# Performance work log

Measured on AMD Instinct MI355X. Metric: run time of the kernel, lower is better.

## Reference

```python
import math
import jax, jax.numpy as jnp
import numpy as np

N, C, T, V = 32, 256, 128, 25
DK, DV, NH = 64, 256, 8
DKH, DVH = DK // NH, DV // NH
EPS = 1e-5


def _spatial_pe(channels, joints):
    # spatial positional encoding: position = joint index, same for all frames
    pos = jnp.arange(joints, dtype=jnp.float32)  # (V,)
    div = jnp.exp(jnp.arange(0, channels, 2, dtype=jnp.float32) * (-math.log(10000.0) / channels))
    ang = pos[:, None] * div[None, :]  # (V, C/2)
    pe = jnp.stack([jnp.sin(ang), jnp.cos(ang)], axis=-1).reshape(joints, channels)  # interleave sin/cos
    return pe.T  # (C, V)


def _qkv_heads(inp, qkv_w, qkv_b):
    # inp: (N, T, C, V); 1x1 conv == channel GEMM
    qkv = jnp.einsum('oc,ntcv->ntov', qkv_w, inp) + qkv_b[None, None, :, None]
    q = qkv[:, :, :DK].reshape(N, T, NH, DKH, V) * (DKH ** -0.5)
    k = qkv[:, :, DK:2 * DK].reshape(N, T, NH, DKH, V)
    g = qkv[:, :, 2 * DK:3 * DK].reshape(N, T, NH, DKH, V)
    v = qkv[:, :, 3 * DK:].reshape(N, T, NH, DVH, V)
    return q, k, g, v


def setup_inputs() -> dict:
    key = jax.random.key(0)
    ks = jax.random.split(key, 3)
    return {
        'x': jax.random.normal(ks[0], (N, C, T, V), dtype=jnp.float32),
        'qkv_w': jax.random.normal(ks[1], (3 * DK + DV, C), dtype=jnp.float32) * 0.02,
        'qkv_b': jnp.zeros((3 * DK + DV,), dtype=jnp.float32),
        'attn_w': jax.random.normal(ks[2], (DV, DV), dtype=jnp.float32) * 0.02,
        'attn_b': jnp.zeros((DV,), dtype=jnp.float32),
        'dbn_gamma': jnp.ones((C * V,), dtype=jnp.float32),
        'dbn_beta': jnp.zeros((C * V,), dtype=jnp.float32),
        'bn_gamma': jnp.ones((DV,), dtype=jnp.float32),
        'bn_beta': jnp.zeros((DV,), dtype=jnp.float32),
    }


def reference(x, qkv_w, qkv_b, attn_w, attn_b, dbn_gamma, dbn_beta, bn_gamma, bn_beta):
    x_sum = x
    pe = _spatial_pe(C, V)  # (C, V)
    pos = x + pe[None, :, None, :]  # broadcast over N, T

    # data_bn: BatchNorm1d over C*V features (training mode, batch stats over N and T)
    xr = x.transpose(0, 1, 3, 2).reshape(N, C * V, T)
    mu = xr.mean(axis=(0, 2))
    var = xr.var(axis=(0, 2))
    xr = (xr - mu[None, :, None]) * jax.lax.rsqrt(var + EPS)[None, :, None]
    xr = xr * dbn_gamma[None, :, None] + dbn_beta[None, :, None]
    xn = xr.reshape(N, C, V, T).transpose(0, 1, 3, 2)  # (N, C, T, V)

    xa = xn.transpose(0, 2, 1, 3)   # (N, T, C, V)
    pa = pos.transpose(0, 2, 1, 3)  # (N, T, C, V)

    q, k, g, v = _qkv_heads(xa, qkv_w, qkv_b)
    pq, pk, _, _ = _qkv_heads(pa, qkv_w, qkv_b)

    mu_q = q.mean(-1, keepdims=True)          # (N,T,Nh,dkh,1)
    qc = q - mu_q
    pairwise = jnp.einsum('nthdv,nthdw->nthvw', qc, k)    # (N,T,Nh,V,V)
    unary = jnp.einsum('nthdv,nthdw->nthvw', mu_q, g)     # (N,T,Nh,1,V)
    lp = jnp.einsum('nthdv,nthdw->nthvw', pq, pk)         # (N,T,Nh,V,V)

    weights = jnp.tanh(pairwise + lp) + jnp.tanh(unary + lp)
    attn = jnp.einsum('nthvw,nthew->nthev', weights, v)   # (N,T,Nh,dvh,V)
    attn = attn.reshape(N, T, DV, V)
    attn = jnp.einsum('oe,ntev->ntov', attn_w, attn) + attn_b[None, None, :, None]
    y = attn.transpose(0, 2, 1, 3) + x_sum  # skip (in_c == out_c)

    # bn: BatchNorm2d over out_c (training mode)
    mu2 = y.mean(axis=(0, 2, 3))
    var2 = y.var(axis=(0, 2, 3))
    y = (y - mu2[None, :, None, None]) * jax.lax.rsqrt(var2 + EPS)[None, :, None, None]
    y = y * bn_gamma[None, :, None, None] + bn_beta[None, :, None, None]
    return jax.nn.relu(y)
```

## Files before the change

### kernel.cpp

```cpp
#include <hip/hip_runtime.h>
#include <hip/hip_bf16.h>
#include <math.h>

#define N_   32
#define C_   256
#define T_   128
#define V_   25
#define CTV  (C_ * T_ * V_)
#define TV   (T_ * V_)
#define EPS_ 1e-5f
#define S_Q  0.35355339059327373f
#define NCOPY 64

typedef __attribute__((ext_vector_type(8))) short bf16x8;
typedef __attribute__((ext_vector_type(4))) float f32x4;
typedef __attribute__((ext_vector_type(4))) unsigned short u16x4;

__device__ inline ushort f2b(float f) {
    __hip_bfloat16 h = __float2bfloat16(f);
    return *reinterpret_cast<ushort*>(&h);
}
__device__ inline float b2f(ushort u) {
    __hip_bfloat16 h;
    *reinterpret_cast<ushort*>(&h) = u;
    return __bfloat162float(h);
}
__device__ inline float tanh_fast(float x) {
    float xc = fminf(fmaxf(x, -12.f), 12.f);
    float e = __expf(xc + xc);
    return (e - 1.f) * __builtin_amdgcn_rcpf(e + 1.f);
}
#define LD8(p) (*(const bf16x8*)(p))
#define MFMA16(a, b, c) __builtin_amdgcn_mfma_f32_16x16x32_bf16(a, b, c, 0, 0, 0)

__device__ inline int qtswz(int v, int col) {
    return v * 320 + ((((col >> 3)) ^ (v & 7)) << 3) + (col & 7);
}
__device__ inline int qvswz(int e, int w) {
    return e * 32 + (((w >> 3) ^ (e & 3)) << 3) + (w & 7);
}
__device__ inline int bswz(int v, int c) {
    return v * 256 + ((((c >> 3) ^ (v & 7)) << 3) | (c & 7));
}

__global__ void prep_kernel(const float* __restrict__ qkv_w,
                            const float* __restrict__ attn_w,
                            ushort* __restrict__ Wq, ushort* __restrict__ Wa,
                            float* __restrict__ pe, float* __restrict__ bins) {
    int idx = blockIdx.x * blockDim.x + threadIdx.x;
    int stride = gridDim.x * blockDim.x;
    for (int i = idx; i < 448 * 256; i += stride) {
        float w = qkv_w[i];
        if (i < 64 * 256) w *= S_Q;
        Wq[i] = f2b(w);
    }
    for (int i = idx; i < 256 * 256; i += stride) Wa[i] = f2b(attn_w[i]);
    for (int i = idx; i < C_ * V_; i += stride) {
        int c = i / V_, v = i - c * V_;
        int j2 = c & ~1;
        float ang = (float)v * expf(-logf(10000.0f) * (float)j2 / (float)C_);
        pe[i] = (c & 1) ? cosf(ang) : sinf(ang);
    }
    for (int i = idx; i < NCOPY * 512; i += stride) bins[i] = 0.f;
}

__global__ __launch_bounds__(1024) void dbn_kernel(const float* __restrict__ x,
                                                   const float* __restrict__ gamma,
                                                   const float* __restrict__ beta,
                                                   float* __restrict__ a_scale,
                                                   float* __restrict__ a_shift) {
    __shared__ float pgS[32][25], pgQ[32][25];
    int c = blockIdx.x;
    int tid = threadIdx.x, g = tid >> 5, l = tid & 31;
    float s = 0.f, s2 = 0.f;
    if (l < 25) {
        const float* base = x + (size_t)g * CTV + c * TV + l;
        #pragma unroll 8
        for (int t = 0; t < 128; ++t) {
            float v = base[t * 25];
            s += v; s2 += v * v;
        }
        pgS[g][l] = s; pgQ[g][l] = s2;
    }
    __syncthreads();
    if (tid < 25) {
        float S = 0.f, Q = 0.f;
        #pragma unroll
        for (int g2 = 0; g2 < 32; ++g2) { S += pgS[g2][tid]; Q += pgQ[g2][tid]; }
        float inv = 1.0f / 4096.0f;
        float mean = S * inv, var = Q * inv - mean * mean;
        int f = c * 25 + tid;
        float sc = rsqrtf(var + EPS_) * gamma[f];
        a_scale[f] = sc;
        a_shift[f] = beta[f] - mean * sc;
    }
}

__global__ void mkbias_kernel(const ushort* __restrict__ Wq,
                              const float* __restrict__ qkv_b,
                              const float* __restrict__ a_shift,
                              const float* __restrict__ pe,
                              float* __restrict__ bias2, float* __restrict__ peproj) {
    int id = blockIdx.x * 256 + threadIdx.x;
    if (id < 11200) {
        int o = id / 25, v = id - o * 25;
        float acc = qkv_b[o] * (o < 64 ? S_Q : 1.f);
        for (int c = 0; c < 256; ++c)
            acc = fmaf(b2f(Wq[o * 256 + c]), a_shift[c * 25 + v], acc);
        bias2[id] = acc;
    } else if (id < 14400) {
        int id2 = id - 11200;
        int r = id2 / 25, v = id2 - r * 25;
        float acc = qkv_b[r] * (r < 64 ? S_Q : 1.f);
        for (int c = 0; c < 256; ++c)
            acc = fmaf(b2f(Wq[r * 256 + c]), pe[c * 25 + v], acc);
        peproj[id2] = acc;
    }
}

__global__ void b2sum_kernel(const float* __restrict__ bias2,
                             float* __restrict__ bias2sum) {
    int o = threadIdx.x;
    float s = 0.f;
    #pragma unroll
    for (int v = 0; v < 25; ++v) s += bias2[o * 25 + v];
    bias2sum[o] = s;
}

__global__ __launch_bounds__(512, 4) void fused_kernel(
        const float* __restrict__ x,
        const ushort* __restrict__ Wq,
        const float* __restrict__ bias2, const float* __restrict__ peproj,
        const float* __restrict__ a_scale, const float* __restrict__ bias2sum,
        const ushort* __restrict__ Wa, const float* __restrict__ attn_b,
        float* __restrict__ out, float* __restrict__ bins) {
    __shared__ __align__(16) char smem[53376];
    ushort* Braw = (ushort*)smem;
    ushort* Bxn  = (ushort*)(smem + 16384);
    ushort* qkvT = (ushort*)(smem + 32768);
    ushort* qkvV = (ushort*)smem;
    ushort* aT   = (ushort*)(smem + 16384);
    ushort* pbuf = (ushort*)(smem + 32768);
    ushort* qmub = (ushort*)(smem + 53248);

    int n = blockIdx.x >> 7, t = blockIdx.x & 127;
    int tid = threadIdx.x, wave = tid >> 6, lane = tid & 63;
    int lr = lane & 15, lg = lane >> 4;
    const float* xp = x + (size_t)n * CTV + t * V_;
    float* outp = out + (size_t)n * CTV + t * V_;
    float* mybins = bins + (blockIdx.x & (NCOPY - 1)) * 512;
    const f32x4 zacc = {0.f, 0.f, 0.f, 0.f};
    const bf16x8 zero8 = {0, 0, 0, 0, 0, 0, 0, 0};

    float b2s[4] = {0.f, 0.f, 0.f, 0.f};
    if (wave < 4) {
        #pragma unroll
        for (int i2 = 0; i2 < 4; ++i2)
            b2s[i2] = bias2sum[wave * 16 + lg * 4 + i2];
    }

    {
        float xv[13], sc[13];
        #pragma unroll
        for (int j = 0; j < 13; ++j) {
            int i = tid + j * 512;
            if (i < 6400) {
                int c = i / 25, v = i - c * 25;
                xv[j] = xp[c * TV + v];
                sc[j] = a_scale[i];
            }
        }
        #pragma unroll
        for (int j = 0; j < 13; ++j) {
            int i = tid + j * 512;
            if (i < 6400) {
                int c = i / 25, v = i - c * 25;
                int off = bswz(v, c);
                Braw[off] = f2b(xv[j]);
                Bxn[off]  = f2b(xv[j] * sc[j]);
            }
        }
        for (int i = tid; i < 448; i += 512) {
            int v = 25 + (i >> 6), c = (i & 63) * 4;
            u16x4 z4 = {0, 0, 0, 0};
            *(u16x4*)(Braw + v * 256 + c) = z4;
            *(u16x4*)(Bxn + v * 256 + c) = z4;
        }
    }
    __syncthreads();

    {
        const ushort* Arow = Wq + (wave * 16 + lr) * 256;
        f32x4 a0 = zacc, a1 = zacc;
        #pragma unroll
        for (int kk = 0; kk < 8; ++kk) {
            int k0 = kk * 32 + lg * 8;
            int oct = (((k0 >> 3) ^ (lr & 7)) << 3);
            bf16x8 a  = LD8(Arow + k0);
            bf16x8 b0 = LD8(Braw + lr * 256 + oct);
            bf16x8 b1 = LD8(Braw + (16 + lr) * 256 + oct);
            a0 = MFMA16(a, b0, a0);
            a1 = MFMA16(a, b1, a1);
        }
        int rb = wave * 16 + lg * 4;
        u16x4 r0, r1;
        #pragma unroll
        for (int i2 = 0; i2 < 4; ++i2) {
            int r = rb + i2;
            r0[i2] = f2b(a0[i2] + peproj[r * 25 + lr]);
            r1[i2] = (lr < 9) ? f2b(a1[i2] + peproj[r * 25 + 16 + lr]) : (ushort)0;
        }
        *(u16x4*)(qkvT + qtswz(lr, 192 + rb)) = r0;
        *(u16x4*)(qkvT + qtswz(16 + lr, 192 + rb)) = r1;
    }
    __syncthreads();

    {
        int myTiles = (wave < 4) ? 4 : 3;
        f32x4 acc[4][2];
        #pragma unroll
        for (int i = 0; i < 4; ++i) { acc[i][0] = zacc; acc[i][1] = zacc; }
        #pragma unroll
        for (int kk = 0; kk < 8; ++kk) {
            int k0 = kk * 32 + lg * 8;
            int oct = (((k0 >> 3) ^ (lr & 7)) << 3);
            bf16x8 b0 = LD8(Bxn + lr * 256 + oct);
            bf16x8 b1 = LD8(Bxn + (16 + lr) * 256 + oct);
            #pragma unroll
            for (int tt = 0; tt < 4; ++tt) {
                if (tt < myTiles) {
                    int mt = wave + tt * 8;
                    bf16x8 a = LD8(Wq + (mt * 16 + lr) * 256 + k0);
                    acc[tt][0] = MFMA16(a, b0, acc[tt][0]);
                    acc[tt][1] = MFMA16(a, b1, acc[tt][1]);
                }
            }
        }
        #pragma unroll
        for (int tt = 0; tt < 4; ++tt) {
            if (tt < myTiles) {
                int mt = wave + tt * 8;
                int ob = mt * 16 + lg * 4;
                if (mt < 4) {
                    u16x4 r0, r1;
                    #pragma unroll
                    for (int i2 = 0; i2 < 4; ++i2) {
                        int o = ob + i2;
                        float cs = acc[tt][0][i2] + ((lr < 9) ? acc[tt][1][i2] : 0.f);
                        #pragma unroll
                        for (int mm = 1; mm < 16; mm <<= 1)
                            cs += __shfl_xor(cs, mm, 64);
                        float mu = (cs + b2s[i2]) * 0.04f;
                        ushort mur = f2b(mu);
                        float muf = b2f(mur);
                        r0[i2] = f2b(acc[tt][0][i2] + bias2[o * 25 + lr] - muf);
                        r1[i2] = (lr < 9)
                            ? f2b(acc[tt][1][i2] + bias2[o * 25 + 16 + lr] - muf)
                            : (ushort)0;
                        if (lr == 0) qmub[o] = mur;
                    }
                    *(u16x4*)(qkvT + qtswz(lr, ob)) = r0;
                    *(u16x4*)(qkvT + qtswz(16 + lr, ob)) = r1;
                } else if (mt < 12) {
                    u16x4 r0, r1;
                    #pragma unroll
                    for (int i2 = 0; i2 < 4; ++i2) {
                        int o = ob + i2;
                        r0[i2] = f2b(acc[tt][0][i2] + bias2[o * 25 + lr]);
                        r1[i2] = (lr < 9)
                            ? f2b(acc[tt][1][i2] + bias2[o * 25 + 16 + lr])
                            : (ushort)0;
                    }
                    *(u16x4*)(qkvT + qtswz(lr, ob)) = r0;
                    *(u16x4*)(qkvT + qtswz(16 + lr, ob)) = r1;
                } else {
                    #pragma unroll
                    for (int i2 = 0; i2 < 4; ++i2) {
                        int o = ob + i2;
                        int e = o - 192;
                        qkvV[qvswz(e, lr)] = f2b(acc[tt][0][i2] + bias2[o * 25 + lr]);
                        qkvV[qvswz(e, 16 + lr)] = (lr < 9)
                            ? f2b(acc[tt][1][i2] + bias2[o * 25 + 16 + lr])
                            : (ushort)0;
                    }
                }
            }
        }
    }
    __syncthreads();

    int h = wave;
    bf16x8 mu8 = LD8(qmub + h * 8);
    bf16x8 aP1[2], aP2[2], bP1[2], bP2[2];
    #pragma unroll
    for (int mi = 0; mi < 2; ++mi) {
        int row = mi * 16 + lr, sx = row & 7;
        const ushort* rp = qkvT + row * 320;
        aP1[mi] = (lg == 0) ? LD8(rp + ((h ^ sx) << 3))
                : (lg == 1) ? LD8(rp + (((24 + h) ^ sx) << 3)) : zero8;
        aP2[mi] = (lg == 0) ? LD8(rp + (((24 + h) ^ sx) << 3))
                : (lg == 1) ? mu8 : zero8;
        bP1[mi] = (lg == 0) ? LD8(rp + (((8 + h) ^ sx) << 3))
                : (lg == 1) ? LD8(rp + (((32 + h) ^ sx) << 3)) : zero8;
        bP2[mi] = (lg == 0) ? LD8(rp + (((32 + h) ^ sx) << 3))
                : (lg == 1) ? LD8(rp + (((16 + h) ^ sx) << 3)) : zero8;
    }
    f32x4 p1[2][2], p2[2][2];
    #pragma unroll
    for (int mi = 0; mi < 2; ++mi)
        #pragma unroll
        for (int ni = 0; ni < 2; ++ni) {
            p1[mi][ni] = MFMA16(aP1[mi], bP1[ni], zacc);
            p2[mi][ni] = MFMA16(aP2[mi], bP2[ni], zacc);
        }
    __syncthreads();

    #pragma unroll
    for (int mi = 0; mi < 2; ++mi)
        #pragma unroll
        for (int ni = 0; ni < 2; ++ni) {
            int w = ni * 16 + lr;
            #pragma unroll
            for (int i2 = 0; i2 < 4; ++i2) {
                int v = mi * 16 + lg * 4 + i2;
                float tw = tanh_fast(p1[mi][ni][i2]) + tanh_fast(p2[mi][ni][i2]);
                pbuf[(h * 32 + v) * 40 + w] = (w < 25) ? f2b(tw) : (ushort)0;
            }
        }

    {
        bf16x8 aw[2], bv[2];
        #pragma unroll
        for (int mi = 0; mi < 2; ++mi)
            aw[mi] = LD8(pbuf + (h * 32 + mi * 16 + lr) * 40 + lg * 8);
        #pragma unroll
        for (int ni = 0; ni < 2; ++ni) {
            int e = h * 32 + ni * 16 + lr;
            bv[ni] = LD8(qkvV + e * 32 + ((lg ^ (e & 3)) << 3));
        }
        f32x4 at_[2][2];
        #pragma unroll
        for (int mi = 0; mi < 2; ++mi)
            #pragma unroll
            for (int ni = 0; ni < 2; ++ni)
                at_[mi][ni] = MFMA16(aw[mi], bv[ni], zacc);
        #pragma unroll
        for (int mi = 0; mi < 2; ++mi)
            #pragma unroll
            for (int ni = 0; ni < 2; ++ni)
                #pragma unroll
                for (int i2 = 0; i2 < 4; ++i2) {
                    int v = mi * 16 + lg * 4 + i2;
                    int e = h * 32 + ni * 16 + lr;
                    if (v < 25) aT[bswz(v, e)] = f2b(at_[mi][ni][i2]);
                }
    }
    __syncthreads();

    float sk0[2][4], sk1[2][4];
    #pragma unroll
    for (int tt = 0; tt < 2; ++tt)
        #pragma unroll
        for (int i2 = 0; i2 < 4; ++i2) {
            int o = (wave + tt * 8) * 16 + lg * 4 + i2;
            sk0[tt][i2] = xp[o * TV + lr];
            sk1[tt][i2] = (lr < 9) ? xp[o * TV + 16 + lr] : 0.f;
        }
    #pragma unroll
    for (int tt = 0; tt < 2; ++tt) {
        int o0 = (wave + tt * 8) * 16;
        const ushort* Arow = Wa + (o0 + lr) * 256;
        f32x4 a0 = zacc, a1 = zacc;
        #pragma unroll
        for (int kk = 0; kk < 8; ++kk) {
            int k0 = kk * 32 + lg * 8;
            int oct = (((k0 >> 3) ^ (lr & 7)) << 3);
            bf16x8 a  = LD8(Arow + k0);
            bf16x8 b0 = LD8(aT + lr * 256 + oct);
            bf16x8 b1 = LD8(aT + (16 + lr) * 256 + oct);
            a0 = MFMA16(a, b0, a0);
            a1 = MFMA16(a, b1, a1);
        }
        #pragma unroll
        for (int i2 = 0; i2 < 4; ++i2) {
            int o = o0 + lg * 4 + i2;
            float bias = attn_b[o];
            float v0 = a0[i2] + bias + sk0[tt][i2];
            outp[o * TV + lr] = v0;
            float v1 = 0.f;
            if (lr < 9) {
                v1 = a1[i2] + bias + sk1[tt][i2];
                outp[o * TV + 16 + lr] = v1;
            }
            float cs = v0 + v1, cq = v0 * v0 + v1 * v1;
            #pragma unroll
            for (int mm = 1; mm < 16; mm <<= 1) {
                cs += __shfl_xor(cs, mm, 64);
                cq += __shfl_xor(cq, mm, 64);
            }
            if (lr == 0) {
                atomicAdd(&mybins[o], cs);
                atomicAdd(&mybins[256 + o], cq);
            }
        }
    }
}

__global__ void bn2_final_kernel(const float* __restrict__ bins,
                                 const float* __restrict__ gamma,
                                 const float* __restrict__ beta,
                                 float* __restrict__ scale,
                                 float* __restrict__ shift) {
    int c = threadIdx.x;
    float s = 0.f, q = 0.f;
    for (int cp = 0; cp < NCOPY; ++cp) {
        s += bins[cp * 512 + c];
        q += bins[cp * 512 + 256 + c];
    }
    float inv = 1.0f / (float)(N_ * TV);
    float mean = s * inv;
    float var = q * inv - mean * mean;
    float sc = rsqrtf(var + EPS_) * gamma[c];
    scale[c] = sc;
    shift[c] = beta[c] - mean * sc;
}

__global__ void bn2_apply_kernel(float4* __restrict__ y,
                                 const float* __restrict__ scale,
                                 const float* __restrict__ shift) {
    const int total4 = N_ * CTV / 4;
    for (int i = blockIdx.x * blockDim.x + threadIdx.x; i < total4;
         i += gridDim.x * blockDim.x) {
        int c = (i / (TV / 4)) & 255;
        float4 v = y[i];
        float sc = scale[c], sh = shift[c];
        v.x = fmaxf(fmaf(v.x, sc, sh), 0.f);
        v.y = fmaxf(fmaf(v.y, sc, sh), 0.f);
        v.z = fmaxf(fmaf(v.z, sc, sh), 0.f);
        v.w = fmaxf(fmaf(v.w, sc, sh), 0.f);
        y[i] = v;
    }
}

extern "C" void kernel_launch(void* const* d_in, const int* in_sizes, int n_in,
                              void* d_out, int out_size, void* d_ws, size_t ws_size,
                              hipStream_t stream) {
    const float* x      = (const float*)d_in[0];
    const float* qkv_w  = (const float*)d_in[1];
    const float* qkv_b  = (const float*)d_in[2];
    const float* attn_w = (const float*)d_in[3];
    const float* attn_b = (const float*)d_in[4];
    const float* dbn_g  = (const float*)d_in[5];
    const float* dbn_b  = (const float*)d_in[6];
    const float* bn_g   = (const float*)d_in[7];
    const float* bn_b   = (const float*)d_in[8];
    float* out = (float*)d_out;

    char* ws = (char*)d_ws;
    ushort* Wq       = (ushort*)ws;
    ushort* Wa       = (ushort*)(ws + 229376);
    float*  pe       = (float*)(ws + 360448);
    float*  a_scale  = (float*)(ws + 386048);
    float*  a_shift  = (float*)(ws + 411648);
    float*  bias2    = (float*)(ws + 437248);
    float*  peproj   = (float*)(ws + 482048);
    float*  bias2sum = (float*)(ws + 494848);
    float*  bins     = (float*)(ws + 495104);
    float*  bn2_sc   = (float*)(ws + 626176);
    float*  bn2_sh   = (float*)(ws + 627200);

    prep_kernel<<<256, 256, 0, stream>>>(qkv_w, attn_w, Wq, Wa, pe, bins);
    dbn_kernel<<<C_, 1024, 0, stream>>>(x, dbn_g, dbn_b, a_scale, a_shift);
    mkbias_kernel<<<57, 256, 0, stream>>>(Wq, qkv_b, a_shift, pe, bias2, peproj);
    b2sum_kernel<<<1, 64, 0, stream>>>(bias2, bias2sum);
    fused_kernel<<<N_ * T_, 512, 0, stream>>>(x, Wq, bias2, peproj, a_scale,
                                              bias2sum, Wa, attn_b, out, bins);
    bn2_final_kernel<<<1, 256, 0, stream>>>(bins, bn_g, bn_b, bn2_sc, bn2_sh);
    bn2_apply_kernel<<<4096, 256, 0, stream>>>((float4*)out, bn2_sc, bn2_sh);
}
```

Measured before the change: 352.8 us.

## Prefetch GEMM weight fragments into registers and drop an intermediate barrier

Weight fragments for the PE projection GEMM are loaded into registers before the input staging phase. The QKV and output-projection GEMMs double-buffer their weight loads one k-step ahead, so global load latency overlaps with MFMA work. The barrier between the PE GEMM and the QKV GEMM is moved to after the QKV accumulation and before the epilogue writes into aliased shared memory. The input staging is also reorganised so each thread reads about 13 contiguous floats of one channel. The trade-off is a large rise in vector register use, which may lower occupancy, and the new per-thread access pattern for the input may coalesce less well.

```diff
diff --git a/kernel.cpp b/kernel.cpp
--- a/kernel.cpp
+++ b/kernel.cpp
@@ -151,7 +151,17 @@
     float* mybins = bins + (blockIdx.x & (NCOPY - 1)) * 512;
     const f32x4 zacc = {0.f, 0.f, 0.f, 0.f};
     const bf16x8 zero8 = {0, 0, 0, 0, 0, 0, 0, 0};
-
+    int myTiles = (wave < 4) ? 4 : 3;
+
+    bf16x8 apk[8];
+    const ushort* Arow0 = Wq + (wave * 16 + lr) * 256;
+    #pragma unroll
+    for (int kk = 0; kk < 8; ++kk) apk[kk] = LD8(Arow0 + kk * 32 + lg * 8);
+    bf16x8 acur[4];
+    #pragma unroll
+    for (int tt = 0; tt < 4; ++tt)
+        if (tt < myTiles)
+            acur[tt] = LD8(Wq + ((wave + tt * 8) * 16 + lr) * 256 + lg * 8);
     float b2s[4] = {0.f, 0.f, 0.f, 0.f};
     if (wave < 4) {
         #pragma unroll
@@ -160,47 +170,40 @@
     }
 
     {
+        int c = tid >> 1, half = tid & 1;
+        int v0 = half * 13, nv = 13 - half;
+        const float* xc = xp + c * TV + v0;
+        const float* scp = a_scale + c * 25 + v0;
         float xv[13], sc[13];
         #pragma unroll
-        for (int j = 0; j < 13; ++j) {
-            int i = tid + j * 512;
-            if (i < 6400) {
-                int c = i / 25, v = i - c * 25;
-                xv[j] = xp[c * TV + v];
-                sc[j] = a_scale[i];
-            }
-        }
-        #pragma unroll
-        for (int j = 0; j < 13; ++j) {
-            int i = tid + j * 512;
-            if (i < 6400) {
-                int c = i / 25, v = i - c * 25;
-                int off = bswz(v, c);
+        for (int j = 0; j < 13; ++j)
+            if (j < nv) { xv[j] = xc[j]; sc[j] = scp[j]; }
+        #pragma unroll
+        for (int j = 0; j < 13; ++j)
+            if (j < nv) {
+                int off = bswz(v0 + j, c);
                 Braw[off] = f2b(xv[j]);
                 Bxn[off]  = f2b(xv[j] * sc[j]);
             }
-        }
         for (int i = tid; i < 448; i += 512) {
-            int v = 25 + (i >> 6), c = (i & 63) * 4;
+            int v = 25 + (i >> 6), cz = (i & 63) * 4;
             u16x4 z4 = {0, 0, 0, 0};
-            *(u16x4*)(Braw + v * 256 + c) = z4;
-            *(u16x4*)(Bxn + v * 256 + c) = z4;
+            *(u16x4*)(Braw + v * 256 + cz) = z4;
+            *(u16x4*)(Bxn + v * 256 + cz) = z4;
         }
     }
     __syncthreads();
 
     {
-        const ushort* Arow = Wq + (wave * 16 + lr) * 256;
         f32x4 a0 = zacc, a1 = zacc;
         #pragma unroll
         for (int kk = 0; kk < 8; ++kk) {
             int k0 = kk * 32 + lg * 8;
             int oct = (((k0 >> 3) ^ (lr & 7)) << 3);
-            bf16x8 a  = LD8(Arow + k0);
             bf16x8 b0 = LD8(Braw + lr * 256 + oct);
             bf16x8 b1 = LD8(Braw + (16 + lr) * 256 + oct);
-            a0 = MFMA16(a, b0, a0);
-            a1 = MFMA16(a, b1, a1);
+            a0 = MFMA16(apk[kk], b0, a0);
+            a1 = MFMA16(apk[kk], b1, a1);
         }
         int rb = wave * 16 + lg * 4;
         u16x4 r0, r1;
@@ -213,15 +216,21 @@
         *(u16x4*)(qkvT + qtswz(lr, 192 + rb)) = r0;
         *(u16x4*)(qkvT + qtswz(16 + lr, 192 + rb)) = r1;
     }
-    __syncthreads();
-
+
+    f32x4 acc[4][2];
+    #pragma unroll
+    for (int i = 0; i < 4; ++i) { acc[i][0] = zacc; acc[i][1] = zacc; }
     {
-        int myTiles = (wave < 4) ? 4 : 3;
-        f32x4 acc[4][2];
-        #pragma unroll
-        for (int i = 0; i < 4; ++i) { acc[i][0] = zacc; acc[i][1] = zacc; }
+        bf16x8 anxt[4];
         #pragma unroll
         for (int kk = 0; kk < 8; ++kk) {
+            if (kk < 7) {
+                #pragma unroll
+                for (int tt = 0; tt < 4; ++tt)
+                    if (tt < myTiles)
+                        anxt[tt] = LD8(Wq + ((wave + tt * 8) * 16 + lr) * 256
+                                       + (kk + 1) * 32 + lg * 8);
+            }
             int k0 = kk * 32 + lg * 8;
             int oct = (((k0 >> 3) ^ (lr & 7)) << 3);
             bf16x8 b0 = LD8(Bxn + lr * 256 + oct);
@@ -229,60 +238,63 @@
             #pragma unroll
             for (int tt = 0; tt < 4; ++tt) {
                 if (tt < myTiles) {
-                    int mt = wave + tt * 8;
-                    bf16x8 a = LD8(Wq + (mt * 16 + lr) * 256 + k0);
-                    acc[tt][0] = MFMA16(a, b0, acc[tt][0]);
-                    acc[tt][1] = MFMA16(a, b1, acc[tt][1]);
+                    acc[tt][0] = MFMA16(acur[tt], b0, acc[tt][0]);
+                    acc[tt][1] = MFMA16(acur[tt], b1, acc[tt][1]);
                 }
             }
-        }
-        #pragma unroll
-        for (int tt = 0; tt < 4; ++tt) {
-            if (tt < myTiles) {
-                int mt = wave + tt * 8;
-                int ob = mt * 16 + lg * 4;
-                if (mt < 4) {
-                    u16x4 r0, r1;
+            #pragma unroll
+            for (int tt = 0; tt < 4; ++tt)
+                if (tt < myTiles) acur[tt] = anxt[tt];
+        }
+    }
+    __syncthreads();
+
+    #pragma unroll
+    for (int tt = 0; tt < 4; ++tt) {
+        if (tt < myTiles) {
+            int mt = wave + tt * 8;
+            int ob = mt * 16 + lg * 4;
+            if (mt < 4) {
+                u16x4 r0, r1;
+                #pragma unroll
+                for (int i2 = 0; i2 < 4; ++i2) {
+                    int o = ob + i2;
+                    float cs = acc[tt][0][i2] + ((lr < 9) ? acc[tt][1][i2] : 0.f);
                     #pragma unroll
-                    for (int i2 = 0; i2 < 4; ++i2) {
-                        int o = ob + i2;
-                        float cs = acc[tt][0][i2] + ((lr < 9) ? acc[tt][1][i2] : 0.f);
-                        #pragma unroll
-                        for (int mm = 1; mm < 16; mm <<= 1)
-                            cs += __shfl_xor(cs, mm, 64);
-                        float mu = (cs + b2s[i2]) * 0.04f;
-                        ushort mur = f2b(mu);
-                        float muf = b2f(mur);
-                        r0[i2] = f2b(acc[tt][0][i2] + bias2[o * 25 + lr] - muf);
-                        r1[i2] = (lr < 9)
-                            ? f2b(acc[tt][1][i2] + bias2[o * 25 + 16 + lr] - muf)
-                            : (ushort)0;
-                        if (lr == 0) qmub[o] = mur;
-                    }
-                    *(u16x4*)(qkvT + qtswz(lr, ob)) = r0;
-                    *(u16x4*)(qkvT + qtswz(16 + lr, ob)) = r1;
-                } else if (mt < 12) {
-                    u16x4 r0, r1;
-                    #pragma unroll
-                    for (int i2 = 0; i2 < 4; ++i2) {
-                        int o = ob + i2;
-                        r0[i2] = f2b(acc[tt][0][i2] + bias2[o * 25 + lr]);
-                        r1[i2] = (lr < 9)
-                            ? f2b(acc[tt][1][i2] + bias2[o * 25 + 16 + lr])
-                            : (ushort)0;
-                    }
-                    *(u16x4*)(qkvT + qtswz(lr, ob)) = r0;
-                    *(u16x4*)(qkvT + qtswz(16 + lr, ob)) = r1;
-                } else {
-                    #pragma unroll
-                    for (int i2 = 0; i2 < 4; ++i2) {
-                        int o = ob + i2;
-                        int e = o - 192;
-                        qkvV[qvswz(e, lr)] = f2b(acc[tt][0][i2] + bias2[o * 25 + lr]);
-                        qkvV[qvswz(e, 16 + lr)] = (lr < 9)
-                            ? f2b(acc[tt][1][i2] + bias2[o * 25 + 16 + lr])
-                            : (ushort)0;
-                    }
+                    for (int mm = 1; mm < 16; mm <<= 1)
+                        cs += __shfl_xor(cs, mm, 64);
+                    float mu = (cs + b2s[i2]) * 0.04f;
+                    ushort mur = f2b(mu);
+                    float muf = b2f(mur);
+                    r0[i2] = f2b(acc[tt][0][i2] + bias2[o * 25 + lr] - muf);
+                    r1[i2] = (lr < 9)
+                        ? f2b(acc[tt][1][i2] + bias2[o * 25 + 16 + lr] - muf)
+                        : (ushort)0;
+                    if (lr == 0) qmub[o] = mur;
+                }
+                *(u16x4*)(qkvT + qtswz(lr, ob)) = r0;
+                *(u16x4*)(qkvT + qtswz(16 + lr, ob)) = r1;
+            } else if (mt < 12) {
+                u16x4 r0, r1;
+                #pragma unroll
+                for (int i2 = 0; i2 < 4; ++i2) {
+                    int o = ob + i2;
+                    r0[i2] = f2b(acc[tt][0][i2] + bias2[o * 25 + lr]);
+                    r1[i2] = (lr < 9)
+                        ? f2b(acc[tt][1][i2] + bias2[o * 25 + 16 + lr])
+                        : (ushort)0;
+                }
+                *(u16x4*)(qkvT + qtswz(lr, ob)) = r0;
+                *(u16x4*)(qkvT + qtswz(16 + lr, ob)) = r1;
+            } else {
+                #pragma unroll
+                for (int i2 = 0; i2 < 4; ++i2) {
+                    int o = ob + i2;
+                    int e = o - 192;
+                    qkvV[qvswz(e, lr)] = f2b(acc[tt][0][i2] + bias2[o * 25 + lr]);
+                    qkvV[qvswz(e, 16 + lr)] = (lr < 9)
+                        ? f2b(acc[tt][1][i2] + bias2[o * 25 + 16 + lr])
+                        : (ushort)0;
                 }
             }
         }
@@ -371,15 +383,17 @@
         int o0 = (wave + tt * 8) * 16;
         const ushort* Arow = Wa + (o0 + lr) * 256;
         f32x4 a0 = zacc, a1 = zacc;
+        bf16x8 wac = LD8(Arow + lg * 8), wan;
         #pragma unroll
         for (int kk = 0; kk < 8; ++kk) {
+            if (kk < 7) wan = LD8(Arow + (kk + 1) * 32 + lg * 8);
             int k0 = kk * 32 + lg * 8;
             int oct = (((k0 >> 3) ^ (lr & 7)) << 3);
-            bf16x8 a  = LD8(Arow + k0);
             bf16x8 b0 = LD8(aT + lr * 256 + oct);
             bf16x8 b1 = LD8(aT + (16 + lr) * 256 + oct);
-            a0 = MFMA16(a, b0, a0);
-            a1 = MFMA16(a, b1, a1);
+            a0 = MFMA16(wac, b0, a0);
+            a1 = MFMA16(wac, b1, a1);
+            wac = wan;
         }
         #pragma unroll
         for (int i2 = 0; i2 < 4; ++i2) {
```

After: 374.4 us. 1.06x slower.

## Shrink LDS footprint by aliasing input buffers to raise block occupancy

Applied to the files above, without the earlier changes.

Cuts shared memory per block from about 53KB to 37KB. Instead of separate raw-x and normalized-x staging buffers, one buffer is reused: raw values are written first, then overwritten with scaled values after the first GEMM. V-projection results are kept in registers until the buffer is free, and extra barriers are added to order the aliased writes. This should let more 512-thread blocks fit per CU, at the cost of extra __syncthreads and more live registers (xv/sc arrays, accV), which could hit the launch-bounds register cap.

```diff
diff --git a/kernel.cpp b/kernel.cpp
--- a/kernel.cpp
+++ b/kernel.cpp
@@ -134,14 +134,13 @@
         const float* __restrict__ a_scale, const float* __restrict__ bias2sum,
         const ushort* __restrict__ Wa, const float* __restrict__ attn_b,
         float* __restrict__ out, float* __restrict__ bins) {
-    __shared__ __align__(16) char smem[53376];
-    ushort* Braw = (ushort*)smem;
-    ushort* Bxn  = (ushort*)(smem + 16384);
-    ushort* qkvT = (ushort*)(smem + 32768);
-    ushort* qkvV = (ushort*)smem;
-    ushort* aT   = (ushort*)(smem + 16384);
-    ushort* pbuf = (ushort*)(smem + 32768);
-    ushort* qmub = (ushort*)(smem + 53248);
+    __shared__ __align__(16) char smem[36992];
+    ushort* qkvT = (ushort*)smem;
+    ushort* pbuf = (ushort*)smem;
+    ushort* Bbuf = (ushort*)(smem + 20480);
+    ushort* qkvV = (ushort*)(smem + 20480);
+    ushort* aT   = (ushort*)(smem + 20480);
+    ushort* qmub = (ushort*)(smem + 36864);
 
     int n = blockIdx.x >> 7, t = blockIdx.x & 127;
     int tid = threadIdx.x, wave = tid >> 6, lane = tid & 63;
@@ -151,6 +150,7 @@
     float* mybins = bins + (blockIdx.x & (NCOPY - 1)) * 512;
     const f32x4 zacc = {0.f, 0.f, 0.f, 0.f};
     const bf16x8 zero8 = {0, 0, 0, 0, 0, 0, 0, 0};
+    int myTiles = (wave < 4) ? 4 : 3;
 
     float b2s[4] = {0.f, 0.f, 0.f, 0.f};
     if (wave < 4) {
@@ -159,8 +159,8 @@
             b2s[i2] = bias2sum[wave * 16 + lg * 4 + i2];
     }
 
+    float xv[13], sc[13];
     {
-        float xv[13], sc[13];
         #pragma unroll
         for (int j = 0; j < 13; ++j) {
             int i = tid + j * 512;
@@ -175,16 +175,13 @@
             int i = tid + j * 512;
             if (i < 6400) {
                 int c = i / 25, v = i - c * 25;
-                int off = bswz(v, c);
-                Braw[off] = f2b(xv[j]);
-                Bxn[off]  = f2b(xv[j] * sc[j]);
+                Bbuf[bswz(v, c)] = f2b(xv[j]);
             }
         }
         for (int i = tid; i < 448; i += 512) {
-            int v = 25 + (i >> 6), c = (i & 63) * 4;
+            int v = 25 + (i >> 6), cz = (i & 63) * 4;
             u16x4 z4 = {0, 0, 0, 0};
-            *(u16x4*)(Braw + v * 256 + c) = z4;
-            *(u16x4*)(Bxn + v * 256 + c) = z4;
+            *(u16x4*)(Bbuf + v * 256 + cz) = z4;
         }
     }
     __syncthreads();
@@ -197,8 +194,8 @@
             int k0 = kk * 32 + lg * 8;
             int oct = (((k0 >> 3) ^ (lr & 7)) << 3);
             bf16x8 a  = LD8(Arow + k0);
-            bf16x8 b0 = LD8(Braw + lr * 256 + oct);
-            bf16x8 b1 = LD8(Braw + (16 + lr) * 256 + oct);
+            bf16x8 b0 = LD8(Bbuf + lr * 256 + oct);
+            bf16x8 b1 = LD8(Bbuf + (16 + lr) * 256 + oct);
             a0 = MFMA16(a, b0, a0);
             a1 = MFMA16(a, b1, a1);
         }
@@ -215,8 +212,19 @@
     }
     __syncthreads();
 
+    #pragma unroll
+    for (int j = 0; j < 13; ++j) {
+        int i = tid + j * 512;
+        if (i < 6400) {
+            int c = i / 25, v = i - c * 25;
+            Bbuf[bswz(v, c)] = f2b(xv[j] * sc[j]);
+        }
+    }
+    __syncthreads();
+
+    f32x4 accV[2][2];
+    int vIdx = 0;
     {
-        int myTiles = (wave < 4) ? 4 : 3;
         f32x4 acc[4][2];
         #pragma unroll
         for (int i = 0; i < 4; ++i) { acc[i][0] = zacc; acc[i][1] = zacc; }
@@ -224,8 +232,8 @@
         for (int kk = 0; kk < 8; ++kk) {
             int k0 = kk * 32 + lg * 8;
             int oct = (((k0 >> 3) ^ (lr & 7)) << 3);
-            bf16x8 b0 = LD8(Bxn + lr * 256 + oct);
-            bf16x8 b1 = LD8(Bxn + (16 + lr) * 256 + oct);
+            bf16x8 b0 = LD8(Bbuf + lr * 256 + oct);
+            bf16x8 b1 = LD8(Bbuf + (16 + lr) * 256 + oct);
             #pragma unroll
             for (int tt = 0; tt < 4; ++tt) {
                 if (tt < myTiles) {
@@ -274,20 +282,37 @@
                     *(u16x4*)(qkvT + qtswz(lr, ob)) = r0;
                     *(u16x4*)(qkvT + qtswz(16 + lr, ob)) = r1;
                 } else {
+                    accV[vIdx][0] = acc[tt][0];
+                    accV[vIdx][1] = acc[tt][1];
+                    ++vIdx;
+                }
+            }
+        }
+    }
+    __syncthreads();
+
+    {
+        int vi = 0;
+        #pragma unroll
+        for (int tt = 0; tt < 4; ++tt) {
+            if (tt < myTiles) {
+                int mt = wave + tt * 8;
+                if (mt >= 12) {
+                    int ob = mt * 16 + lg * 4;
                     #pragma unroll
                     for (int i2 = 0; i2 < 4; ++i2) {
                         int o = ob + i2;
                         int e = o - 192;
-                        qkvV[qvswz(e, lr)] = f2b(acc[tt][0][i2] + bias2[o * 25 + lr]);
+                        qkvV[qvswz(e, lr)] = f2b(accV[vi][0][i2] + bias2[o * 25 + lr]);
                         qkvV[qvswz(e, 16 + lr)] = (lr < 9)
-                            ? f2b(acc[tt][1][i2] + bias2[o * 25 + 16 + lr])
+                            ? f2b(accV[vi][1][i2] + bias2[o * 25 + 16 + lr])
                             : (ushort)0;
                     }
+                    ++vi;
                 }
             }
         }
     }
-    __syncthreads();
 
     int h = wave;
     bf16x8 mu8 = LD8(qmub + h * 8);
@@ -327,7 +352,7 @@
                 pbuf[(h * 32 + v) * 40 + w] = (w < 25) ? f2b(tw) : (ushort)0;
             }
         }
-
+    f32x4 at_[2][2];
     {
         bf16x8 aw[2], bv[2];
         #pragma unroll
@@ -338,23 +363,24 @@
             int e = h * 32 + ni * 16 + lr;
             bv[ni] = LD8(qkvV + e * 32 + ((lg ^ (e & 3)) << 3));
         }
-        f32x4 at_[2][2];
         #pragma unroll
         for (int mi = 0; mi < 2; ++mi)
             #pragma unroll
             for (int ni = 0; ni < 2; ++ni)
                 at_[mi][ni] = MFMA16(aw[mi], bv[ni], zacc);
-        #pragma unroll
-        for (int mi = 0; mi < 2; ++mi)
+    }
+    __syncthreads();
+
+    #pragma unroll
+    for (int mi = 0; mi < 2; ++mi)
+        #pragma unroll
+        for (int ni = 0; ni < 2; ++ni)
             #pragma unroll
-            for (int ni = 0; ni < 2; ++ni)
-                #pragma unroll
-                for (int i2 = 0; i2 < 4; ++i2) {
-                    int v = mi * 16 + lg * 4 + i2;
-                    int e = h * 32 + ni * 16 + lr;
-                    if (v < 25) aT[bswz(v, e)] = f2b(at_[mi][ni][i2]);
-                }
-    }
+            for (int i2 = 0; i2 < 4; ++i2) {
+                int v = mi * 16 + lg * 4 + i2;
+                int e = h * 32 + ni * 16 + lr;
+                if (v < 25) aT[bswz(v, e)] = f2b(at_[mi][ni][i2]);
+            }
     __syncthreads();
 
     float sk0[2][4], sk1[2][4];
```

Measured after the change: 386.4 us. +9.5%, slower.

## Split fused attention kernel into transpose, GEMM, attention and GEMM stages

Applied to the files above, without the earlier changes.

Replaces the single per-(n,t) fused kernel with four kernels: a transpose/convert of x into bf16 channel-last buffers, a tiled QKV projection GEMM over 64-column tiles, a per-frame attention kernel, and a tiled output GEMM that also accumulates BN statistics. The goal is better weight reuse and larger GEMM tiles than the per-frame blocks allow. In exchange it adds large intermediate round trips through global memory (about 185 MB of workspace, with the output buffer reused as scratch) and an extra zeroing pass over the V buffer. The old fused path is kept as a fallback when the workspace is too small.

```diff
diff --git a/kernel.cpp b/kernel.cpp
--- a/kernel.cpp
+++ b/kernel.cpp
@@ -46,7 +46,8 @@
 __global__ void prep_kernel(const float* __restrict__ qkv_w,
                             const float* __restrict__ attn_w,
                             ushort* __restrict__ Wq, ushort* __restrict__ Wa,
-                            float* __restrict__ pe, float* __restrict__ bins) {
+                            float* __restrict__ pe, float* __restrict__ bins,
+                            ushort* __restrict__ vout, int zero_vout) {
     int idx = blockIdx.x * blockDim.x + threadIdx.x;
     int stride = gridDim.x * blockDim.x;
     for (int i = idx; i < 448 * 256; i += stride) {
@@ -62,6 +63,11 @@
         pe[i] = (c & 1) ? cosf(ang) : sinf(ang);
     }
     for (int i = idx; i < NCOPY * 512; i += stride) bins[i] = 0.f;
+    if (zero_vout) {
+        u16x4 z = {0, 0, 0, 0};
+        u16x4* vp = (u16x4*)vout;
+        for (int i = idx; i < 32 * 128 * 256 * 8; i += stride) vp[i] = z;
+    }
 }
 
 __global__ __launch_bounds__(1024) void dbn_kernel(const float* __restrict__ x,
@@ -127,7 +133,246 @@
     bias2sum[o] = s;
 }
 
-__global__ __launch_bounds__(512, 4) void fused_kernel(
+__global__ __launch_bounds__(256) void prepx_kernel(const float* __restrict__ x,
+                                                    const float* __restrict__ a_scale,
+                                                    ushort* __restrict__ xnT,
+                                                    ushort* __restrict__ xrawT) {
+    __shared__ float tile[64][65];
+    int nt = blockIdx.x, ct = blockIdx.y, n = blockIdx.z;
+    int tid = threadIdx.x;
+    const float* xb = x + (size_t)n * CTV + ct * 64 * TV + nt * 64;
+    #pragma unroll
+    for (int it = 0; it < 16; ++it) {
+        int idx = it * 256 + tid;
+        int cc = idx >> 6, tv = idx & 63;
+        tile[cc][tv] = xb[cc * TV + tv];
+    }
+    __syncthreads();
+    #pragma unroll
+    for (int it = 0; it < 16; ++it) {
+        int idx = it * 256 + tid;
+        int tv = idx >> 6, cc = idx & 63;
+        int gtv = nt * 64 + tv, gc = ct * 64 + cc;
+        float xv = tile[cc][tv];
+        size_t off = ((size_t)n * 3200 + gtv) * 256 + gc;
+        xrawT[off] = f2b(xv);
+        xnT[off] = f2b(xv * a_scale[gc * 25 + gtv % 25]);
+    }
+}
+
+__global__ __launch_bounds__(256) void gemm1_kernel(
+        const ushort* __restrict__ xnT, const ushort* __restrict__ xrawT,
+        const ushort* __restrict__ Wq,
+        const float* __restrict__ bias2, const float* __restrict__ peproj,
+        ushort* __restrict__ qkvT_g, ushort* __restrict__ vout) {
+    int nt = blockIdx.x, mt = blockIdx.y, n = blockIdx.z;
+    int tid = threadIdx.x, wave = tid >> 6, lane = tid & 63;
+    int lr = lane & 15, lg = lane >> 4;
+    const f32x4 zacc = {0.f, 0.f, 0.f, 0.f};
+    bool pos = (mt >= 7);
+    int rbase = mt * 64 + wave * 16;
+    int wrow = pos ? rbase - 448 : rbase;
+    const ushort* Arow = Wq + (wrow + lr) * 256;
+    const ushort* Bbase = (pos ? xrawT : xnT) + ((size_t)n * 3200 + nt * 64) * 256;
+    f32x4 acc[4];
+    acc[0] = zacc; acc[1] = zacc; acc[2] = zacc; acc[3] = zacc;
+    #pragma unroll
+    for (int kk = 0; kk < 8; ++kk) {
+        int k0 = kk * 32 + lg * 8;
+        bf16x8 a = LD8(Arow + k0);
+        #pragma unroll
+        for (int ni = 0; ni < 4; ++ni) {
+            bf16x8 b = LD8(Bbase + (ni * 16 + lr) * 256 + k0);
+            acc[ni] = MFMA16(a, b, acc[ni]);
+        }
+    }
+    #pragma unroll
+    for (int ni = 0; ni < 4; ++ni) {
+        int col = nt * 64 + ni * 16 + lr;
+        int v = col % 25;
+        int rb = rbase + lg * 4;
+        if (mt <= 2 || pos) {
+            int qcol = pos ? rb - 256 : rb;
+            u16x4 r4;
+            #pragma unroll
+            for (int i2 = 0; i2 < 4; ++i2) {
+                float bsv = pos ? peproj[(rb - 448 + i2) * 25 + v]
+                                : bias2[(rb + i2) * 25 + v];
+                r4[i2] = f2b(acc[ni][i2] + bsv);
+            }
+            *(u16x4*)(qkvT_g + ((size_t)n * 3200 + col) * 320 + qcol) = r4;
+        } else {
+            int t = col / 25;
+            #pragma unroll
+            for (int i2 = 0; i2 < 4; ++i2) {
+                int e = rb - 192 + i2;
+                vout[(((size_t)n * 128 + t) * 256 + e) * 32 + v] =
+                    f2b(acc[ni][i2] + bias2[(rb + i2) * 25 + v]);
+            }
+        }
+    }
+}
+
+__global__ __launch_bounds__(512) void attnmid_kernel(
+        const ushort* __restrict__ qkvT_g, const ushort* __restrict__ vout,
+        ushort* __restrict__ attnT_g) {
+    __shared__ __align__(16) char smem[20736];
+    ushort* qslice = (ushort*)smem;
+    ushort* pbuf = (ushort*)smem;
+    ushort* qmub = (ushort*)(smem + 20480);
+    int blk = blockIdx.x;
+    int n = blk >> 7, t = blk & 127;
+    int tid = threadIdx.x, wave = tid >> 6, lane = tid & 63;
+    int lr = lane & 15, lg = lane >> 4;
+    const f32x4 zacc = {0.f, 0.f, 0.f, 0.f};
+    const bf16x8 zero8 = {0, 0, 0, 0, 0, 0, 0, 0};
+    size_t tvbase = (size_t)n * 3200 + t * 25;
+
+    for (int i = tid; i < 2000; i += 512) {
+        int v = i / 80, c4 = (i - v * 80) * 4;
+        *(u16x4*)(qslice + qtswz(v, c4)) =
+            *(const u16x4*)(qkvT_g + (tvbase + v) * 320 + c4);
+    }
+    for (int i = tid; i < 560; i += 512) {
+        int v = 25 + i / 80, c4 = (i % 80) * 4;
+        u16x4 z = {0, 0, 0, 0};
+        *(u16x4*)(qslice + qtswz(v, c4)) = z;
+    }
+    __syncthreads();
+
+    int h = wave;
+    if (lane < 8) {
+        int o = h * 8 + lane;
+        float s = 0.f;
+        #pragma unroll
+        for (int v = 0; v < 25; ++v)
+            s += b2f(qslice[v * 320 + (((o >> 3) ^ (v & 7)) << 3) + (o & 7)]);
+        s *= (1.f / 25.f);
+        qmub[o] = f2b(s);
+        qmub[64 + o] = f2b(-s);
+    }
+    __syncthreads();
+
+    bf16x8 mu8 = LD8(qmub + h * 8);
+    bf16x8 mun8 = LD8(qmub + 64 + h * 8);
+    bf16x8 aP1[2], aP2[2], bP1[2], bP2[2];
+    #pragma unroll
+    for (int mi = 0; mi < 2; ++mi) {
+        int row = mi * 16 + lr, sx = row & 7;
+        const ushort* rp = qslice + row * 320;
+        aP1[mi] = (lg == 0) ? LD8(rp + ((h ^ sx) << 3))
+                : (lg == 1) ? LD8(rp + (((24 + h) ^ sx) << 3))
+                : (lg == 2) ? mun8 : zero8;
+        bP1[mi] = (lg == 0) ? LD8(rp + (((8 + h) ^ sx) << 3))
+                : (lg == 1) ? LD8(rp + (((32 + h) ^ sx) << 3))
+                : (lg == 2) ? LD8(rp + (((8 + h) ^ sx) << 3)) : zero8;
+        aP2[mi] = (lg == 0) ? LD8(rp + (((24 + h) ^ sx) << 3))
+                : (lg == 1) ? mu8 : zero8;
+        bP2[mi] = (lg == 0) ? LD8(rp + (((32 + h) ^ sx) << 3))
+                : (lg == 1) ? LD8(rp + (((16 + h) ^ sx) << 3)) : zero8;
+    }
+    f32x4 p1[2][2], p2[2][2];
+    #pragma unroll
+    for (int mi = 0; mi < 2; ++mi)
+        #pragma unroll
+        for (int ni = 0; ni < 2; ++ni) {
+            p1[mi][ni] = MFMA16(aP1[mi], bP1[ni], zacc);
+            p2[mi][ni] = MFMA16(aP2[mi], bP2[ni], zacc);
+        }
+    __syncthreads();
+
+    #pragma unroll
+    for (int mi = 0; mi < 2; ++mi)
+        #pragma unroll
+        for (int ni = 0; ni < 2; ++ni) {
+            int w = ni * 16 + lr;
+            #pragma unroll
+            for (int i2 = 0; i2 < 4; ++i2) {
+                int v = mi * 16 + lg * 4 + i2;
+                float tw = tanh_fast(p1[mi][ni][i2]) + tanh_fast(p2[mi][ni][i2]);
+                pbuf[(h * 32 + v) * 40 + w] = (w < 25) ? f2b(tw) : (ushort)0;
+            }
+        }
+
+    f32x4 at_[2][2];
+    {
+        bf16x8 aw[2], bv[2];
+        #pragma unroll
+        for (int mi = 0; mi < 2; ++mi)
+            aw[mi] = LD8(pbuf + (h * 32 + mi * 16 + lr) * 40 + lg * 8);
+        #pragma unroll
+        for (int ni = 0; ni < 2; ++ni) {
+            int e = h * 32 + ni * 16 + lr;
+            bv[ni] = LD8(vout + (((size_t)n * 128 + t) * 256 + e) * 32 + lg * 8);
+        }
+        #pragma unroll
+        for (int mi = 0; mi < 2; ++mi)
+            #pragma unroll
+            for (int ni = 0; ni < 2; ++ni)
+                at_[mi][ni] = MFMA16(aw[mi], bv[ni], zacc);
+    }
+    #pragma unroll
+    for (int mi = 0; mi < 2; ++mi)
+        #pragma unroll
+        for (int ni = 0; ni < 2; ++ni)
+            #pragma unroll
+            for (int i2 = 0; i2 < 4; ++i2) {
+                int v = mi * 16 + lg * 4 + i2;
+                int e = h * 32 + ni * 16 + lr;
+                if (v < 25) attnT_g[(tvbase + v) * 256 + e] = f2b(at_[mi][ni][i2]);
+            }
+}
+
+__global__ __launch_bounds__(256) void gemm2_kernel(
+        const ushort* __restrict__ Wa, const ushort* __restrict__ attnT_g,
+        const float* __restrict__ attn_b, const float* __restrict__ x,
+        float* __restrict__ out, float* __restrict__ bins) {
+    int nt = blockIdx.x, mt = blockIdx.y, n = blockIdx.z;
+    int tid = threadIdx.x, wave = tid >> 6, lane = tid & 63;
+    int lr = lane & 15, lg = lane >> 4;
+    const f32x4 zacc = {0.f, 0.f, 0.f, 0.f};
+    int o_base = mt * 64 + wave * 16;
+    const ushort* Arow = Wa + (o_base + lr) * 256;
+    const ushort* Bbase = attnT_g + ((size_t)n * 3200 + nt * 64) * 256;
+    f32x4 acc[4];
+    acc[0] = zacc; acc[1] = zacc; acc[2] = zacc; acc[3] = zacc;
+    #pragma unroll
+    for (int kk = 0; kk < 8; ++kk) {
+        int k0 = kk * 32 + lg * 8;
+        bf16x8 a = LD8(Arow + k0);
+        #pragma unroll
+        for (int ni = 0; ni < 4; ++ni) {
+            bf16x8 b = LD8(Bbase + (ni * 16 + lr) * 256 + k0);
+            acc[ni] = MFMA16(a, b, acc[ni]);
+        }
+    }
+    float* mybins = bins + ((nt + mt * 50 + n * 200) & (NCOPY - 1)) * 512;
+    #pragma unroll
+    for (int i2 = 0; i2 < 4; ++i2) {
+        int o = o_base + lg * 4 + i2;
+        float bias = attn_b[o];
+        float cs = 0.f, cq = 0.f;
+        #pragma unroll
+        for (int ni = 0; ni < 4; ++ni) {
+            int col = nt * 64 + ni * 16 + lr;
+            size_t off = ((size_t)n * 256 + o) * 3200 + col;
+            float v0 = acc[ni][i2] + bias + x[off];
+            out[off] = v0;
+            cs += v0; cq += v0 * v0;
+        }
+        #pragma unroll
+        for (int mm = 1; mm < 16; mm <<= 1) {
+            cs += __shfl_xor(cs, mm, 64);
+            cq += __shfl_xor(cq, mm, 64);
+        }
+        if (lr == 0) {
+            atomicAdd(&mybins[o], cs);
+            atomicAdd(&mybins[256 + o], cq);
+        }
+    }
+}
+
+__global__ __launch_bounds__(512, 4) void fused_kernel_fb(
         const float* __restrict__ x,
         const ushort* __restrict__ Wq,
         const float* __restrict__ bias2, const float* __restrict__ peproj,
@@ -158,7 +403,6 @@
         for (int i2 = 0; i2 < 4; ++i2)
             b2s[i2] = bias2sum[wave * 16 + lg * 4 + i2];
     }
-
     {
         float xv[13], sc[13];
         #pragma unroll
@@ -181,14 +425,13 @@
             }
         }
         for (int i = tid; i < 448; i += 512) {
-            int v = 25 + (i >> 6), c = (i & 63) * 4;
+            int v = 25 + (i >> 6), cz = (i & 63) * 4;
             u16x4 z4 = {0, 0, 0, 0};
-            *(u16x4*)(Braw + v * 256 + c) = z4;
-            *(u16x4*)(Bxn + v * 256 + c) = z4;
-        }
-    }
-    __syncthreads();
-
+            *(u16x4*)(Braw + v * 256 + cz) = z4;
+            *(u16x4*)(Bxn + v * 256 + cz) = z4;
+        }
+    }
+    __syncthreads();
     {
         const ushort* Arow = Wq + (wave * 16 + lr) * 256;
         f32x4 a0 = zacc, a1 = zacc;
@@ -214,7 +457,6 @@
         *(u16x4*)(qkvT + qtswz(16 + lr, 192 + rb)) = r1;
     }
     __syncthreads();
-
     {
         int myTiles = (wave < 4) ? 4 : 3;
         f32x4 acc[4][2];
@@ -288,7 +530,6 @@
         }
     }
     __syncthreads();
-
     int h = wave;
     bf16x8 mu8 = LD8(qmub + h * 8);
     bf16x8 aP1[2], aP2[2], bP1[2], bP2[2];
@@ -314,7 +555,6 @@
             p2[mi][ni] = MFMA16(aP2[mi], bP2[ni], zacc);
         }
     __syncthreads();
-
     #pragma unroll
     for (int mi = 0; mi < 2; ++mi)
         #pragma unroll
@@ -327,7 +567,6 @@
                 pbuf[(h * 32 + v) * 40 + w] = (w < 25) ? f2b(tw) : (ushort)0;
             }
         }
-
     {
         bf16x8 aw[2], bv[2];
         #pragma unroll
@@ -356,7 +595,6 @@
                 }
     }
     __syncthreads();
-
     float sk0[2][4], sk1[2][4];
     #pragma unroll
     for (int tt = 0; tt < 2; ++tt)
@@ -468,13 +706,32 @@
     float*  bins     = (float*)(ws + 495104);
     float*  bn2_sc   = (float*)(ws + 626176);
     float*  bn2_sh   = (float*)(ws + 627200);
-
-    prep_kernel<<<256, 256, 0, stream>>>(qkv_w, attn_w, Wq, Wa, pe, bins);
+    ushort* qkvT_g   = (ushort*)(ws + 628224);
+    ushort* voutg    = (ushort*)(ws + 66164224);
+    ushort* attnT_g  = (ushort*)(ws + 133273088);
+    const size_t NEEDED = 185701888;
+
+    bool big = (ws_size >= NEEDED);
+
+    prep_kernel<<<256, 256, 0, stream>>>(qkv_w, attn_w, Wq, Wa, pe, bins,
+                                         voutg, big ? 1 : 0);
     dbn_kernel<<<C_, 1024, 0, stream>>>(x, dbn_g, dbn_b, a_scale, a_shift);
     mkbias_kernel<<<57, 256, 0, stream>>>(Wq, qkv_b, a_shift, pe, bias2, peproj);
-    b2sum_kernel<<<1, 64, 0, stream>>>(bias2, bias2sum);
-    fused_kernel<<<N_ * T_, 512, 0, stream>>>(x, Wq, bias2, peproj, a_scale,
-                                              bias2sum, Wa, attn_b, out, bins);
+
+    if (big) {
+        ushort* xnT = (ushort*)d_out;
+        ushort* xrawT = xnT + 26214400;
+        prepx_kernel<<<dim3(50, 4, 32), 256, 0, stream>>>(x, a_scale, xnT, xrawT);
+        gemm1_kernel<<<dim3(50, 9, 32), 256, 0, stream>>>(xnT, xrawT, Wq, bias2,
+                                                          peproj, qkvT_g, voutg);
+        attnmid_kernel<<<N_ * T_, 512, 0, stream>>>(qkvT_g, voutg, attnT_g);
+        gemm2_kernel<<<dim3(50, 4, 32), 256, 0, stream>>>(Wa, attnT_g, attn_b,
+                                                          x, out, bins);
+    } else {
+        b2sum_kernel<<<1, 64, 0, stream>>>(bias2, bias2sum);
+        fused_kernel_fb<<<N_ * T_, 512, 0, stream>>>(x, Wq, bias2, peproj, a_scale,
+                                                     bias2sum, Wa, attn_b, out, bins);
+    }
     bn2_final_kernel<<<1, 256, 0, stream>>>(bins, bn_g, bn_b, bn2_sc, bn2_sh);
     bn2_apply_kernel<<<4096, 256, 0, stream>>>((float4*)out, bn2_sc, bn2_sh);
 }
```

After: 599.2 us. 69.8% more time.
